# Optimization experiments

Measured on AMD Instinct MI355X. Metric: run time of the kernel, lower is better.

Reference implementation:

```python
import jax, jax.numpy as jnp
import numpy as np

POINTS = 29


def setup_inputs() -> dict:
    key = jax.random.key(0)
    ks = jax.random.split(key, 7)
    B, C, H, W = 16, 128, 64, 64
    S = H * W
    return {
        "data": jax.random.normal(ks[0], (B, C, H, W), dtype=jnp.float32),
        "iscale": jax.random.normal(ks[1], (1, 1, 1, 1), dtype=jnp.float32),
        "oscale": jax.random.normal(ks[2], (1, 1, 1, 1), dtype=jnp.float32),
        "weight_sp": jax.random.normal(ks[3], (1, S, POINTS), dtype=jnp.float32),
        "weight_ch": jax.random.normal(ks[4], (1, C, POINTS), dtype=jnp.float32),
        "conv_w": jax.random.normal(ks[5], (C, C, 3, 3), dtype=jnp.float32) * 0.02,
        "conv_b": jax.random.normal(ks[6], (C,), dtype=jnp.float32) * 0.02,
    }


def _forward(data, iscale, oscale, weight_sp, weight_ch, conv_w, conv_b):
    B, C, H, W = data.shape
    S = H * W
    P = POINTS
    theta_tab = jnp.linspace(-jnp.pi, jnp.pi, P, dtype=data.dtype)
    vel_tab = jnp.linspace(0.0, float(np.e), P, dtype=data.dtype)

    def integral(dflat, param, index):
        # dflat: (B*C*H*W,) flattened normalized input
        d = dflat.reshape(B, C, S)
        # bmm(data, weight_sp) -> (B,C,P), permuted to (B,P,C)
        ch_w = jnp.einsum('bcs,sp->bpc', d, weight_sp[0])
        # bmm(data^T, weight_ch) -> (B,S,P)
        sp_w = jnp.einsum('bcs,cp->bsp', d, weight_ch[0])
        x = jax.lax.conv_general_dilated(
            dflat.reshape(B, C, H, W), conv_w, (1, 1), 'SAME',
            dimension_numbers=('NCHW', 'OIHW', 'NCHW')) + conv_b[None, :, None, None]
        # (B,P,C) @ (B,C,S) @ (B,S,P) -> (B,P,P)
        w = jnp.einsum('bpc,bcs,bsq->bpq', ch_w, x.reshape(B, C, S), sp_w)
        sm = jax.nn.softmax(w.reshape(-1, P), axis=1)  # (B*P, P)
        # sum(param[idx,None] * sm[idx,:], axis=1) == param[idx] * rowsum(sm)[idx]
        rowsum = sm.sum(axis=1)  # (B*P,)
        return param[index] * rowsum[index]

    def interplot(dflat, param, index):
        lmt = param.shape[0] - 1
        p0 = jnp.floor(index).astype(jnp.int32)
        pos = index - p0.astype(index.dtype)
        p0c = jnp.clip(p0, 0, lmt)
        p1c = jnp.clip(p0 + 1, 0, lmt)
        v0 = integral(dflat, param, p0c)
        v1 = integral(dflat, param, p1c)
        return (1.0 - pos) * v0 + pos * v1

    d = (data - data.mean()) / data.std(ddof=1) * iscale  # torch .std() is unbiased
    dflat = d.reshape(-1)
    theta = interplot(dflat, theta_tab, jax.nn.sigmoid(dflat) * (P - 1))
    ds = interplot(dflat, vel_tab, jnp.abs(jnp.tanh(dflat) * (P - 1)))
    dx = ds * jnp.cos(theta)
    dy = ds * jnp.sin(theta)
    out = dflat * jnp.exp(dy) + dx
    out = (out - out.mean()) / out.std(ddof=1)
    return out.reshape(B, C, H, W) * oscale


def reference(data, iscale, oscale, weight_sp, weight_ch, conv_w, conv_b):
    return _forward(data, iscale, oscale, weight_sp, weight_ch, conv_w, conv_b)
```

## Files before the change

### kernel.cpp

```cpp
#include <hip/hip_runtime.h>
#include <math.h>


#define NTOT 8388608
#define NV   (NTOT / 4)
#define GA   1024
#define TB   256
#define STRIDE (GA * TB)
#define ITERS  (NV / STRIDE)

__device__ __forceinline__ float fast_rcp(float x) {
    return __builtin_amdgcn_rcpf(x);
}

__device__ __forceinline__ float lnon_elem(float x, float m1, float k1) {
    float d  = (x - m1) * k1;
    float a  = fminf(fabsf(d), 30.0f);
    float Ea = __expf(a);
    float sg = (d >= 0.0f ? Ea : 1.0f) * fast_rcp(1.0f + Ea);
    float t  = 1.0f - 2.0f * fast_rcp(1.0f + Ea * Ea);
    float dsv = 2.71828182845904523f * t;
    float sn = -__builtin_amdgcn_sinf(sg);
    float cs = -__builtin_amdgcn_cosf(sg);
    return fmaf(d, __expf(dsv * sn), dsv * cs);
}

__device__ __forceinline__ void block_reduce4(double& s1, double& q1,
                                              double& s2, double& q2) {
    #pragma unroll
    for (int off = 32; off > 0; off >>= 1) {
        s1 += __shfl_down(s1, off);
        q1 += __shfl_down(q1, off);
        s2 += __shfl_down(s2, off);
        q2 += __shfl_down(q2, off);
    }
    __shared__ double lds[4][4];
    const int wave = threadIdx.x >> 6;
    const int lane = threadIdx.x & 63;
    __syncthreads();
    if (lane == 0) {
        lds[wave][0] = s1; lds[wave][1] = q1;
        lds[wave][2] = s2; lds[wave][3] = q2;
    }
    __syncthreads();
    s1 = lds[0][0] + lds[1][0] + lds[2][0] + lds[3][0];
    q1 = lds[0][1] + lds[1][1] + lds[2][1] + lds[3][1];
    s2 = lds[0][2] + lds[1][2] + lds[2][2] + lds[3][2];
    q2 = lds[0][3] + lds[1][3] + lds[2][3] + lds[3][3];
}

__global__ __launch_bounds__(TB) void k_p1(const float4* __restrict__ in,
                                           double2* __restrict__ P1) {
    const int t = blockIdx.x * TB + threadIdx.x;
    float s = 0.0f, q = 0.0f;
    #pragma unroll
    for (int k = 0; k < ITERS; ++k) {
        float4 v = in[t + k * STRIDE];
        s += v.x + v.y + v.z + v.w;
        q += v.x * v.x + v.y * v.y + v.z * v.z + v.w * v.w;
    }
    double s1 = (double)s, q1 = (double)q, z2 = 0.0, z3 = 0.0;
    block_reduce4(s1, q1, z2, z3);
    if (threadIdx.x == 0) P1[blockIdx.x] = make_double2(s1, q1);
}

__device__ __forceinline__ void stats_from(double s, double q, float sc,
                                           float& m, float& k) {
    const double Nd = (double)NTOT;
    double mean = s / Nd;
    double var  = (q - s * s / Nd) / (Nd - 1.0);
    m = (float)mean;
    k = (float)(1.0 / sqrt(var)) * sc;
}

__global__ __launch_bounds__(TB) void k_p2(const float4* __restrict__ in,
                                           const float* __restrict__ iscale,
                                           const double2* __restrict__ P1,
                                           double2* __restrict__ P2) {
    double s1 = 0.0, q1 = 0.0, s2 = 0.0, q2 = 0.0;
    #pragma unroll
    for (int i = threadIdx.x; i < GA; i += TB) {
        double2 p = P1[i];
        s1 += p.x; q1 += p.y;
    }
    block_reduce4(s1, q1, s2, q2);
    float m1, k1;
    stats_from(s1, q1, iscale[0], m1, k1);

    const int t = blockIdx.x * TB + threadIdx.x;
    float s = 0.0f, q = 0.0f;
    #pragma unroll
    for (int k = 0; k < ITERS; ++k) {
        float4 v = in[t + k * STRIDE];
        float p0 = lnon_elem(v.x, m1, k1);
        float p1 = lnon_elem(v.y, m1, k1);
        float p2 = lnon_elem(v.z, m1, k1);
        float p3 = lnon_elem(v.w, m1, k1);
        s += p0 + p1 + p2 + p3;
        q += p0 * p0 + p1 * p1 + p2 * p2 + p3 * p3;
    }
    double a = (double)s, b = (double)q, z2 = 0.0, z3 = 0.0;
    block_reduce4(a, b, z2, z3);
    if (threadIdx.x == 0) P2[blockIdx.x] = make_double2(a, b);
}

__global__ __launch_bounds__(TB) void k_p3(const float4* __restrict__ in,
                                           const float* __restrict__ iscale,
                                           const float* __restrict__ oscale,
                                           const double2* __restrict__ P1,
                                           const double2* __restrict__ P2,
                                           float4* __restrict__ out) {
    double s1 = 0.0, q1 = 0.0, s2 = 0.0, q2 = 0.0;
    #pragma unroll
    for (int i = threadIdx.x; i < GA; i += TB) {
        double2 p = P1[i];
        double2 r = P2[i];
        s1 += p.x; q1 += p.y;
        s2 += r.x; q2 += r.y;
    }
    block_reduce4(s1, q1, s2, q2);
    float m1, k1, m2, k2;
    stats_from(s1, q1, iscale[0], m1, k1);
    stats_from(s2, q2, oscale[0], m2, k2);

    const int t = blockIdx.x * TB + threadIdx.x;
    #pragma unroll
    for (int k = 0; k < ITERS; ++k) {
        float4 v = in[t + k * STRIDE];
        float4 o;
        o.x = (lnon_elem(v.x, m1, k1) - m2) * k2;
        o.y = (lnon_elem(v.y, m1, k1) - m2) * k2;
        o.z = (lnon_elem(v.z, m1, k1) - m2) * k2;
        o.w = (lnon_elem(v.w, m1, k1) - m2) * k2;
        out[t + k * STRIDE] = o;
    }
}

extern "C" void kernel_launch(void* const* d_in, const int* in_sizes, int n_in,
                              void* d_out, int out_size, void* d_ws, size_t ws_size,
                              hipStream_t stream) {
    const float4* data   = (const float4*)d_in[0];
    const float*  iscale = (const float*)d_in[1];
    const float*  oscale = (const float*)d_in[2];
    float4* out = (float4*)d_out;
    double2* P1 = (double2*)d_ws;
    double2* P2 = P1 + GA;

    hipLaunchKernelGGL(k_p1, dim3(GA), dim3(TB), 0, stream, data, P1);
    hipLaunchKernelGGL(k_p2, dim3(GA), dim3(TB), 0, stream, data, iscale, P1, P2);
    hipLaunchKernelGGL(k_p3, dim3(GA), dim3(TB), 0, stream, data, iscale, oscale,
                       P1, P2, out);
}
```

Measured before the change: 114.1 us.

## Fuse three passes into one cooperative kernel with register-resident data

Replaces the three separate kernels with one cooperative kernel that uses grid-wide syncs between the statistic phases. Each thread keeps its slice of the input in registers, so the input is read from global memory once instead of three times. The elementwise nonlinearity is also computed once and reused for the final normalisation. The cost is two grid barriers, higher register pressure from holding the tile, and a requirement that all 1024 blocks be co-resident (launch bounds set to 4 blocks per CU).

```diff
diff --git a/kernel.cpp b/kernel.cpp
--- a/kernel.cpp
+++ b/kernel.cpp
@@ -1,5 +1,8 @@
 #include <hip/hip_runtime.h>
+#include <hip/hip_cooperative_groups.h>
 #include <math.h>
+
+namespace cg = cooperative_groups;
 
 
 #define NTOT 8388608
@@ -25,43 +28,20 @@
     return fmaf(d, __expf(dsv * sn), dsv * cs);
 }
 
-__device__ __forceinline__ void block_reduce4(double& s1, double& q1,
-                                              double& s2, double& q2) {
+__device__ __forceinline__ void block_reduce2(double& s, double& q) {
     #pragma unroll
     for (int off = 32; off > 0; off >>= 1) {
-        s1 += __shfl_down(s1, off);
-        q1 += __shfl_down(q1, off);
-        s2 += __shfl_down(s2, off);
-        q2 += __shfl_down(q2, off);
+        s += __shfl_down(s, off);
+        q += __shfl_down(q, off);
     }
-    __shared__ double lds[4][4];
+    __shared__ double lds[4][2];
     const int wave = threadIdx.x >> 6;
     const int lane = threadIdx.x & 63;
     __syncthreads();
-    if (lane == 0) {
-        lds[wave][0] = s1; lds[wave][1] = q1;
-        lds[wave][2] = s2; lds[wave][3] = q2;
-    }
+    if (lane == 0) { lds[wave][0] = s; lds[wave][1] = q; }
     __syncthreads();
-    s1 = lds[0][0] + lds[1][0] + lds[2][0] + lds[3][0];
-    q1 = lds[0][1] + lds[1][1] + lds[2][1] + lds[3][1];
-    s2 = lds[0][2] + lds[1][2] + lds[2][2] + lds[3][2];
-    q2 = lds[0][3] + lds[1][3] + lds[2][3] + lds[3][3];
-}
-
-__global__ __launch_bounds__(TB) void k_p1(const float4* __restrict__ in,
-                                           double2* __restrict__ P1) {
-    const int t = blockIdx.x * TB + threadIdx.x;
-    float s = 0.0f, q = 0.0f;
-    #pragma unroll
-    for (int k = 0; k < ITERS; ++k) {
-        float4 v = in[t + k * STRIDE];
-        s += v.x + v.y + v.z + v.w;
-        q += v.x * v.x + v.y * v.y + v.z * v.z + v.w * v.w;
-    }
-    double s1 = (double)s, q1 = (double)q, z2 = 0.0, z3 = 0.0;
-    block_reduce4(s1, q1, z2, z3);
-    if (threadIdx.x == 0) P1[blockIdx.x] = make_double2(s1, q1);
+    s = lds[0][0] + lds[1][0] + lds[2][0] + lds[3][0];
+    q = lds[0][1] + lds[1][1] + lds[2][1] + lds[3][1];
 }
 
 __device__ __forceinline__ void stats_from(double s, double q, float sc,
@@ -73,65 +53,73 @@
     k = (float)(1.0 / sqrt(var)) * sc;
 }
 
-__global__ __launch_bounds__(TB) void k_p2(const float4* __restrict__ in,
-                                           const float* __restrict__ iscale,
-                                           const double2* __restrict__ P1,
-                                           double2* __restrict__ P2) {
-    double s1 = 0.0, q1 = 0.0, s2 = 0.0, q2 = 0.0;
+__global__ __launch_bounds__(TB, 4) void k_fused(
+        const float4* __restrict__ in,
+        const float*  __restrict__ iscale,
+        const float*  __restrict__ oscale,
+        double2*      __restrict__ P1,
+        double2*      __restrict__ P2,
+        float4*       __restrict__ out) {
+    cg::grid_group grid = cg::this_grid();
+    const int t = blockIdx.x * TB + threadIdx.x;
+
+    float4 v[ITERS];
+    float sf = 0.0f, qf = 0.0f;
+    #pragma unroll
+    for (int k = 0; k < ITERS; ++k) {
+        v[k] = in[t + k * STRIDE];
+        sf += v[k].x + v[k].y + v[k].z + v[k].w;
+        qf += v[k].x * v[k].x + v[k].y * v[k].y
+            + v[k].z * v[k].z + v[k].w * v[k].w;
+    }
+    double s1 = (double)sf, q1 = (double)qf;
+    block_reduce2(s1, q1);
+    if (threadIdx.x == 0) P1[blockIdx.x] = make_double2(s1, q1);
+    grid.sync();
+
+    s1 = 0.0; q1 = 0.0;
     #pragma unroll
     for (int i = threadIdx.x; i < GA; i += TB) {
         double2 p = P1[i];
         s1 += p.x; q1 += p.y;
     }
-    block_reduce4(s1, q1, s2, q2);
+    block_reduce2(s1, q1);
     float m1, k1;
     stats_from(s1, q1, iscale[0], m1, k1);
 
-    const int t = blockIdx.x * TB + threadIdx.x;
-    float s = 0.0f, q = 0.0f;
+    float s2f = 0.0f, q2f = 0.0f;
     #pragma unroll
     for (int k = 0; k < ITERS; ++k) {
-        float4 v = in[t + k * STRIDE];
-        float p0 = lnon_elem(v.x, m1, k1);
-        float p1 = lnon_elem(v.y, m1, k1);
-        float p2 = lnon_elem(v.z, m1, k1);
-        float p3 = lnon_elem(v.w, m1, k1);
-        s += p0 + p1 + p2 + p3;
-        q += p0 * p0 + p1 * p1 + p2 * p2 + p3 * p3;
+        v[k].x = lnon_elem(v[k].x, m1, k1);
+        v[k].y = lnon_elem(v[k].y, m1, k1);
+        v[k].z = lnon_elem(v[k].z, m1, k1);
+        v[k].w = lnon_elem(v[k].w, m1, k1);
+        s2f += v[k].x + v[k].y + v[k].z + v[k].w;
+        q2f += v[k].x * v[k].x + v[k].y * v[k].y
+             + v[k].z * v[k].z + v[k].w * v[k].w;
     }
-    double a = (double)s, b = (double)q, z2 = 0.0, z3 = 0.0;
-    block_reduce4(a, b, z2, z3);
-    if (threadIdx.x == 0) P2[blockIdx.x] = make_double2(a, b);
-}
+    double s2 = (double)s2f, q2 = (double)q2f;
+    block_reduce2(s2, q2);
+    if (threadIdx.x == 0) P2[blockIdx.x] = make_double2(s2, q2);
+    grid.sync();
 
-__global__ __launch_bounds__(TB) void k_p3(const float4* __restrict__ in,
-                                           const float* __restrict__ iscale,
-                                           const float* __restrict__ oscale,
-                                           const double2* __restrict__ P1,
-                                           const double2* __restrict__ P2,
-                                           float4* __restrict__ out) {
-    double s1 = 0.0, q1 = 0.0, s2 = 0.0, q2 = 0.0;
+    s2 = 0.0; q2 = 0.0;
     #pragma unroll
     for (int i = threadIdx.x; i < GA; i += TB) {
-        double2 p = P1[i];
-        double2 r = P2[i];
-        s1 += p.x; q1 += p.y;
-        s2 += r.x; q2 += r.y;
+        double2 p = P2[i];
+        s2 += p.x; q2 += p.y;
     }
-    block_reduce4(s1, q1, s2, q2);
-    float m1, k1, m2, k2;
-    stats_from(s1, q1, iscale[0], m1, k1);
+    block_reduce2(s2, q2);
+    float m2, k2;
     stats_from(s2, q2, oscale[0], m2, k2);
 
-    const int t = blockIdx.x * TB + threadIdx.x;
     #pragma unroll
     for (int k = 0; k < ITERS; ++k) {
-        float4 v = in[t + k * STRIDE];
         float4 o;
-        o.x = (lnon_elem(v.x, m1, k1) - m2) * k2;
-        o.y = (lnon_elem(v.y, m1, k1) - m2) * k2;
-        o.z = (lnon_elem(v.z, m1, k1) - m2) * k2;
-        o.w = (lnon_elem(v.w, m1, k1) - m2) * k2;
+        o.x = (v[k].x - m2) * k2;
+        o.y = (v[k].y - m2) * k2;
+        o.z = (v[k].z - m2) * k2;
+        o.w = (v[k].w - m2) * k2;
         out[t + k * STRIDE] = o;
     }
 }
@@ -142,12 +130,12 @@
     const float4* data   = (const float4*)d_in[0];
     const float*  iscale = (const float*)d_in[1];
     const float*  oscale = (const float*)d_in[2];
-    float4* out = (float4*)d_out;
-    double2* P1 = (double2*)d_ws;
-    double2* P2 = P1 + GA;
+    float4*  out = (float4*)d_out;
+    double2* P1  = (double2*)d_ws;
+    double2* P2  = P1 + GA;
 
-    hipLaunchKernelGGL(k_p1, dim3(GA), dim3(TB), 0, stream, data, P1);
-    hipLaunchKernelGGL(k_p2, dim3(GA), dim3(TB), 0, stream, data, iscale, P1, P2);
-    hipLaunchKernelGGL(k_p3, dim3(GA), dim3(TB), 0, stream, data, iscale, oscale,
-                       P1, P2, out);
+    void* args[] = {(void*)&data, (void*)&iscale, (void*)&oscale,
+                    (void*)&P1, (void*)&P2, (void*)&out};
+    (void)hipLaunchCooperativeKernel((void*)k_fused, dim3(GA), dim3(TB),
+                                     args, 0, stream);
 }
```

Measured after the change: 273.4 us. 2.4x slower.
